# Kernel tuning notes

Measured on AMD Instinct MI355X. Metric: run time of the kernel, lower is better.

## Reference

```python
import jax, jax.numpy as jnp
import numpy as np

N_TOKEN = 267735
CUTOFF_ENDS = [0, 20000, 40000, 200000, N_TOKEN]
DIV_VAL = 4
D_MODEL = 1024
N_HEAD = 16
D_HEAD = 64
D_INNER = 4096
N_LAYER = 4
QLEN = 512
MLEN = 512
BSZ = 4
EPS = 1e-5


def setup_inputs() -> dict:
    key = jax.random.key(0)
    ks = iter(jax.random.split(key, 40))
    std = 0.02
    inp = {}
    inp["input_ids"] = jax.random.randint(next(ks), (BSZ, QLEN), 0, N_TOKEN)
    inp["mems"] = jax.random.normal(next(ks), (N_LAYER, MLEN, BSZ, D_MODEL), jnp.float32) * std
    # adaptive embedding tables + projections (div_val=4 buckets)
    for i in range(4):
        n = CUTOFF_ENDS[i + 1] - CUTOFF_ENDS[i]
        d = D_MODEL // DIV_VAL ** i
        inp[f"emb{i}"] = jax.random.normal(next(ks), (n, d), jnp.float32) * std
        inp[f"proj{i}"] = jax.random.normal(next(ks), (d, D_MODEL), jnp.float32) * std
    L = N_LAYER
    inp["qkv_w"] = jax.random.normal(next(ks), (L, D_MODEL, 3 * N_HEAD * D_HEAD), jnp.float32) * std
    inp["r_net_w"] = jax.random.normal(next(ks), (L, D_MODEL, N_HEAD * D_HEAD), jnp.float32) * std
    inp["o_w"] = jax.random.normal(next(ks), (L, N_HEAD * D_HEAD, D_MODEL), jnp.float32) * std
    inp["r_w_bias"] = jax.random.normal(next(ks), (L, N_HEAD, D_HEAD), jnp.float32) * std
    inp["r_r_bias"] = jax.random.normal(next(ks), (L, N_HEAD, D_HEAD), jnp.float32) * std
    inp["ln1_g"] = jnp.ones((L, D_MODEL), jnp.float32)
    inp["ln1_b"] = jnp.zeros((L, D_MODEL), jnp.float32)
    inp["ff_w1"] = jax.random.normal(next(ks), (L, D_MODEL, D_INNER), jnp.float32) * std
    inp["ff_b1"] = jnp.zeros((L, D_INNER), jnp.float32)
    inp["ff_w2"] = jax.random.normal(next(ks), (L, D_INNER, D_MODEL), jnp.float32) * std
    inp["ff_b2"] = jnp.zeros((L, D_MODEL), jnp.float32)
    inp["ln2_g"] = jnp.ones((L, D_MODEL), jnp.float32)
    inp["ln2_b"] = jnp.zeros((L, D_MODEL), jnp.float32)
    return inp


def _layer_norm(x, g, b):
    m = x.mean(-1, keepdims=True)
    v = ((x - m) ** 2).mean(-1, keepdims=True)
    return (x - m) * jax.lax.rsqrt(v + EPS) * g + b


def _rel_shift(x):
    # x: (qlen, klen, bsz, n_head)
    q, k, b, n = x.shape
    x = jnp.pad(x, ((0, 0), (1, 0), (0, 0), (0, 0)))
    x = x.reshape(k + 1, q, b, n)[1:]
    return x.reshape(q, k, b, n)


def _adaptive_embed(flat_ids, tables_projs):
    emb = jnp.zeros((flat_ids.shape[0], D_MODEL), jnp.float32)
    for i, (tab, proj) in enumerate(tables_projs):
        l, r = CUTOFF_ENDS[i], CUTOFF_ENDS[i + 1]
        mask = (flat_ids >= l) & (flat_ids < r)
        idx = jnp.clip(flat_ids - l, 0, r - l - 1)
        emb = emb + jnp.where(mask[:, None], tab[idx] @ proj, 0.0)
    return emb * (D_MODEL ** 0.5)


def _forward(input_ids, mems, tables_projs, qkv_w, r_net_w, o_w, r_w_bias, r_r_bias,
             ln1_g, ln1_b, ff_w1, ff_b1, ff_w2, ff_b2, ln2_g, ln2_b):
    ids = input_ids.T  # (qlen, bsz)
    word_emb = _adaptive_embed(ids.reshape(-1), tables_projs).reshape(QLEN, BSZ, D_MODEL)

    klen = MLEN + QLEN
    # masked positions == 1: future tokens only (strictly upper triangular over the q part)
    dec_attn_mask = jnp.concatenate(
        [jnp.zeros((QLEN, MLEN), jnp.float32), jnp.triu(jnp.ones((QLEN, QLEN), jnp.float32), 1)], axis=1
    )[:, :, None, None]  # (qlen, klen, 1, 1)

    pos_seq = jnp.arange(klen - 1, -1, -1, dtype=jnp.float32)
    inv_freq = 1.0 / (10000.0 ** (jnp.arange(0, D_MODEL, 2, dtype=jnp.float32) / D_MODEL))
    sin_inp = pos_seq[:, None] * inv_freq[None, :]
    pos_emb = jnp.concatenate([jnp.sin(sin_inp), jnp.cos(sin_inp)], axis=-1)  # (klen, d_model)

    scale = 1.0 / (D_HEAD ** 0.5)
    h = word_emb
    for l in range(N_LAYER):
        cat = jnp.concatenate([mems[l], h], axis=0)              # (klen, bsz, d)
        w_heads = cat @ qkv_w[l]                                  # (klen, bsz, 3*nh*dh)
        wq, wk, wv = jnp.split(w_heads, 3, axis=-1)
        q = wq[-QLEN:].reshape(QLEN, BSZ, N_HEAD, D_HEAD)
        k = wk.reshape(klen, BSZ, N_HEAD, D_HEAD)
        v = wv.reshape(klen, BSZ, N_HEAD, D_HEAD)
        rk = (pos_emb @ r_net_w[l]).reshape(klen, N_HEAD, D_HEAD)
        AC = jnp.einsum('ibnd,jbnd->ijbn', q + r_w_bias[l], k)
        BD = _rel_shift(jnp.einsum('ibnd,jnd->ijbn', q + r_r_bias[l], rk))
        score = (AC + BD) * scale
        score = score * (1.0 - dec_attn_mask) - 1e30 * dec_attn_mask
        prob = jax.nn.softmax(score, axis=1)
        attn_vec = jnp.einsum('ijbn,jbnd->ibnd', prob, v).reshape(QLEN, BSZ, N_HEAD * D_HEAD)
        h = _layer_norm(h + attn_vec @ o_w[l], ln1_g[l], ln1_b[l])
        core = jax.nn.relu(h @ ff_w1[l] + ff_b1[l]) @ ff_w2[l] + ff_b2[l]
        h = _layer_norm(h + core, ln2_g[l], ln2_b[l])
    return jnp.transpose(h, (1, 0, 2))  # (bsz, qlen, d_model)


def reference(input_ids, mems, emb0, proj0, emb1, proj1, emb2, proj2, emb3, proj3,
              qkv_w, r_net_w, o_w, r_w_bias, r_r_bias, ln1_g, ln1_b,
              ff_w1, ff_b1, ff_w2, ff_b2, ln2_g, ln2_b):
    tables_projs = [(emb0, proj0), (emb1, proj1), (emb2, proj2), (emb3, proj3)]
    return _forward(input_ids, mems, tables_projs, qkv_w, r_net_w, o_w, r_w_bias, r_r_bias,
                    ln1_g, ln1_b, ff_w1, ff_b1, ff_w2, ff_b2, ln2_g, ln2_b)
```

## Files before the change

### kernel.cpp

```cpp
#include <hip/hip_runtime.h>
#include <hip/hip_bf16.h>

typedef __attribute__((ext_vector_type(8))) short short8;
typedef __attribute__((ext_vector_type(4))) float f32x4;
typedef __hip_bfloat16 bf16;

#define QLEN 512
#define MLEN 512
#define KLEN 1024
#define BSZ  4
#define DM   1024
#define NH   16
#define DH   64
#define DI   4096
#define NL   4
#define KEMB 1408

__device__ __forceinline__ void gload16(const bf16* g, const void* l) {
  __builtin_amdgcn_global_load_lds(
      (const __attribute__((address_space(1))) void*)g,
      (__attribute__((address_space(3))) void*)l, 16, 0, 0);
}

__device__ __forceinline__ bf16 bits2bf(short s) { bf16 h; *(short*)&h = s; return h; }

__global__ __launch_bounds__(256) void embA_kernel(
    const int* __restrict__ ids,
    const float* __restrict__ e0, const float* __restrict__ e1,
    const float* __restrict__ e2, const float* __restrict__ e3,
    bf16* __restrict__ Aemb)
{
  const int t = blockIdx.x;
  const int q = t >> 2, b = t & 3;
  const int id = ids[b * QLEN + q];
  const float* tab; int d, off, koff;
  if (id < 20000)       { tab = e0; d = 1024; off = 0;      koff = 0; }
  else if (id < 40000)  { tab = e1; d = 256;  off = 20000;  koff = 1024; }
  else if (id < 200000) { tab = e2; d = 64;   off = 40000;  koff = 1280; }
  else                  { tab = e3; d = 16;   off = 200000; koff = 1344; }
  bf16* row = Aemb + (long)t * KEMB;
  const float* tr = tab + (long)(id - off) * d;
  for (int k = threadIdx.x; k < KEMB; k += 256) {
    const int kk = k - koff;
    float v = 0.f;
    if (kk >= 0 && kk < d) v = tr[kk];
    row[k] = __float2bfloat16(v);
  }
}

__global__ __launch_bounds__(256) void projT_kernel(
    const float* __restrict__ p0, const float* __restrict__ p1,
    const float* __restrict__ p2, const float* __restrict__ p3,
    bf16* __restrict__ out)
{
  __shared__ float t[32][33];
  const int k0 = blockIdx.x * 32, n0 = blockIdx.y * 32;
  const int nx = threadIdx.x & 31, ky = threadIdx.x >> 5;
#pragma unroll
  for (int p = 0; p < 4; ++p) {
    const int k = k0 + ky + p * 8;
    float v = 0.f;
    if (k < 1024)       v = p0[(long)k * 1024 + n0 + nx];
    else if (k < 1280)  v = p1[(long)(k - 1024) * 1024 + n0 + nx];
    else if (k < 1344)  v = p2[(long)(k - 1280) * 1024 + n0 + nx];
    else if (k < 1360)  v = p3[(long)(k - 1344) * 1024 + n0 + nx];
    t[ky + p * 8][nx] = v;
  }
  __syncthreads();
#pragma unroll
  for (int p = 0; p < 4; ++p)
    out[(long)(n0 + ky + p * 8) * KEMB + k0 + nx] = __float2bfloat16(t[nx][ky + p * 8]);
}

__global__ __launch_bounds__(256) void embsum_kernel(const float* __restrict__ part,
                                                     float* __restrict__ h, bf16* __restrict__ cat)
{
  const long i = ((long)blockIdx.x * 256 + threadIdx.x) * 4;
  const float4 a = *(const float4*)(part + i);
  const float4 b = *(const float4*)(part + 2097152 + i);
  float4 s; s.x = a.x + b.x; s.y = a.y + b.y; s.z = a.z + b.z; s.w = a.w + b.w;
  *(float4*)(h + i) = s;
  bf16* cr = cat + (long)2048 * 1024 + i;
  cr[0] = __float2bfloat16(s.x); cr[1] = __float2bfloat16(s.y);
  cr[2] = __float2bfloat16(s.z); cr[3] = __float2bfloat16(s.w);
}

__global__ __launch_bounds__(256) void posemb_kernel(bf16* __restrict__ pe)
{
  const int j = blockIdx.x;
  const float pos = (float)(KLEN - 1 - j);
  for (int i = threadIdx.x; i < DM / 2; i += 256) {
    const float freq = expf(-9.210340371976184f * ((float)(2 * i) / (float)DM));
    const float ang = pos * freq;
    pe[(long)j * DM + i]          = __float2bfloat16(sinf(ang));
    pe[(long)j * DM + DM / 2 + i] = __float2bfloat16(cosf(ang));
  }
}

__global__ __launch_bounds__(256) void wtrans_kernel(const float* __restrict__ in,
                                                     bf16* __restrict__ out, int R, int C)
{
  __shared__ float t[32][33];
  in  += (long)blockIdx.z * R * C;
  out += (long)blockIdx.z * R * C;
  const int c0 = blockIdx.x * 32, r0 = blockIdx.y * 32;
  const int cx = threadIdx.x & 31, ry = threadIdx.x >> 5;
#pragma unroll
  for (int p = 0; p < 4; ++p)
    t[ry + p * 8][cx] = in[(long)(r0 + ry + p * 8) * C + c0 + cx];
  __syncthreads();
#pragma unroll
  for (int p = 0; p < 4; ++p)
    out[(long)(c0 + ry + p * 8) * R + r0 + cx] = __float2bfloat16(t[cx][ry + p * 8]);
}

__global__ __launch_bounds__(256) void memsconv_kernel(const float* __restrict__ mems,
                                                       bf16* __restrict__ cat0)
{
  const long i = ((long)blockIdx.x * 256 + threadIdx.x) * 4;
  const long l = i >> 21, rem = i & ((1 << 21) - 1);
  const float4 v = *(const float4*)(mems + i);
  bf16* dst = cat0 + l * 4194304 + rem;
  dst[0] = __float2bfloat16(v.x); dst[1] = __float2bfloat16(v.y);
  dst[2] = __float2bfloat16(v.z); dst[3] = __float2bfloat16(v.w);
}

template<int BM, int BN>
__global__ __launch_bounds__(256) void gemm_bf16(
    const bf16* __restrict__ A, long aStrB, long aStrN, int lda,
    const bf16* __restrict__ B, long bStrB, long bStrN, int ldb,
    void* __restrict__ C, long cStrB, long cStrN, int ldc,
    int K, float scale, const float* __restrict__ bias, long biasStrB, long biasStrN,
    int flags, int zN, int zSplit, long cSplitStr)
{
  constexpr int RA = BM / 64, RB = BN / 64, FM = BM / 32, FN = BN / 32;
  __shared__ __align__(16) bf16 As[2][BM * 32];
  __shared__ __align__(16) bf16 Bs[2][BN * 32];
  const int zc = blockIdx.z % zSplit, zt = blockIdx.z / zSplit;
  const int zn = zt % zN, zb = zt / zN;
  A += (long)zb * aStrB + (long)zn * aStrN + (long)zc * K;
  B += (long)zb * bStrB + (long)zn * bStrN + (long)zc * K;
  const int tid = threadIdx.x, lane = tid & 63;
  const int w = tid >> 6, wr = w >> 1, wc = w & 1;
  const int m0 = blockIdx.y * BM, n0 = blockIdx.x * BN;
  const int l15 = lane & 15, l4 = lane >> 4;
  const int rowS = tid >> 2;
  const int cbS  = (tid & 3) * 16;
  const int swS  = cbS ^ (((rowS >> 1) & 3) << 4);
  const int wbase = w * 1024;
  const bf16* Ast = A + (size_t)(m0 + rowS) * lda + (swS >> 1);
  const bf16* Bst = B + (size_t)(n0 + rowS) * ldb + (swS >> 1);

#define STAGE_TILE(buf, kk)                                                       \
  {                                                                               \
    _Pragma("unroll")                                                             \
    for (int r = 0; r < RA; ++r)                                                  \
      gload16(Ast + (size_t)(r * 64) * lda + (kk), (char*)As[buf] + r * 4096 + wbase); \
    _Pragma("unroll")                                                             \
    for (int r = 0; r < RB; ++r)                                                  \
      gload16(Bst + (size_t)(r * 64) * ldb + (kk), (char*)Bs[buf] + r * 4096 + wbase); \
  }

  f32x4 acc[FM][FN] = {};
  STAGE_TILE(0, 0)
  asm volatile("s_waitcnt vmcnt(0)" ::: "memory");
  __syncthreads();
  int cur = 0;
  for (int k0 = 0; k0 < K; k0 += 32) {
    if (k0 + 32 < K) {
      if (cur == 0) STAGE_TILE(1, k0 + 32)
      else          STAGE_TILE(0, k0 + 32)
    }
    short8 af[FM], bfr[FN];
#pragma unroll
    for (int f = 0; f < FM; ++f) {
      const int row = wr * (BM / 2) + f * 16 + l15;
      af[f] = *(const short8*)((char*)As[cur] + row * 64 + ((16 * l4) ^ (((row >> 1) & 3) << 4)));
    }
#pragma unroll
    for (int f = 0; f < FN; ++f) {
      const int row = wc * (BN / 2) + f * 16 + l15;
      bfr[f] = *(const short8*)((char*)Bs[cur] + row * 64 + ((16 * l4) ^ (((row >> 1) & 3) << 4)));
    }
#pragma unroll
    for (int fm = 0; fm < FM; ++fm)
#pragma unroll
      for (int fn = 0; fn < FN; ++fn)
        acc[fm][fn] = __builtin_amdgcn_mfma_f32_16x16x32_bf16(af[fm], bfr[fn], acc[fm][fn], 0, 0, 0);
    asm volatile("s_waitcnt vmcnt(0)" ::: "memory");
    __syncthreads();
    cur ^= 1;
  }
#undef STAGE_TILE
  const int outbf = flags & 1, relu = flags & 4;
#pragma unroll
  for (int fm = 0; fm < FM; ++fm) {
#pragma unroll
    for (int fn = 0; fn < FN; ++fn) {
      const int col = n0 + wc * (BN / 2) + fn * 16 + l15;
      const int rw0 = m0 + wr * (BM / 2) + fm * 16 + l4 * 4;
      const float bv = (bias && zc == 0) ? bias[(size_t)zb * biasStrB + (size_t)zn * biasStrN + col] : 0.f;
#pragma unroll
      for (int r = 0; r < 4; ++r) {
        float v = (acc[fm][fn][r] + bv) * scale;
        if (relu) v = fmaxf(v, 0.f);
        const int row = rw0 + r;
        const size_t cOff = (size_t)zb * cStrB + (size_t)zn * cStrN + (size_t)zc * cSplitStr;
        if (outbf) {
          ((bf16*)C + cOff)[(size_t)row * ldc + col] = __float2bfloat16(v);
        } else {
          ((float*)C + cOff)[(size_t)row * ldc + col] = v;
        }
      }
    }
  }
}

__global__ __launch_bounds__(256) void vt_kernel(const bf16* __restrict__ wh,
                                                 bf16* __restrict__ vt, bf16* __restrict__ kb)
{
  const int bn = blockIdx.y, b = bn >> 4, n = bn & 15;
  const int j0 = blockIdx.x * 64;
  __shared__ bf16 t[64][72];
  const bf16* src = wh + (size_t)b * 3072 + 2048 + n * 64;
  const bf16* ksrc = wh + (size_t)b * 3072 + 1024 + n * 64;
  bf16* kdst = kb + (size_t)bn * 65536;
  const int tid = threadIdx.x;
#pragma unroll
  for (int r = 0; r < 16; ++r) {
    const int jl = r * 4 + (tid >> 6), d = tid & 63;
    t[jl][d] = src[(size_t)(j0 + jl) * 12288 + d];
    kdst[(size_t)(j0 + jl) * 64 + d] = ksrc[(size_t)(j0 + jl) * 12288 + d];
  }
  __syncthreads();
  bf16* dst = vt + (size_t)bn * 64 * KLEN;
#pragma unroll
  for (int r = 0; r < 16; ++r) {
    const int d = r * 4 + (tid >> 6), j = tid & 63;
    dst[(size_t)d * KLEN + j0 + j] = t[j][d];
  }
}

__global__ __launch_bounds__(256) void fattn_kernel(
    const bf16* __restrict__ wh,
    const bf16* __restrict__ kb,
    const bf16* __restrict__ rkb_l,
    const bf16* __restrict__ vt,
    const float* __restrict__ rwb,
    const float* __restrict__ rrb,
    float* __restrict__ po, float* __restrict__ pm, float* __restrict__ pl)
{
  const int bn = blockIdx.x, b = bn >> 4, n = bn & 15;
  const int q0 = blockIdx.y * 64;
  const int ck = blockIdx.z;
  const int tid = threadIdx.x, w = tid >> 6, lane = tid & 63;
  const int l15 = lane & 15, l4 = lane >> 4;
  __shared__ bf16 Tl[4][16][84];
  __shared__ bf16 Pl[4][16][72];

  short8 qa[2], qb[2];
  {
    const bf16* qp = wh + (size_t)(2048 + b) * 3072 + (size_t)(q0 + 16 * w + l15) * 12288 + n * 64;
#pragma unroll
    for (int kk = 0; kk < 2; ++kk) {
      const short8 qv = *(const short8*)(qp + kk * 32 + 8 * l4);
      const float* wv = rwb + n * 64 + kk * 32 + 8 * l4;
      const float* rv = rrb + n * 64 + kk * 32 + 8 * l4;
      short8 a, c;
#pragma unroll
      for (int e = 0; e < 8; ++e) {
        const float q = __bfloat162float(bits2bf(qv[e]));
        const bf16 ab = __float2bfloat16((q + wv[e]) * 0.125f);
        const bf16 cb = __float2bfloat16((q + rv[e]) * 0.125f);
        a[e] = *(const short*)&ab;  c[e] = *(const short*)&cb;
      }
      qa[kk] = a; qb[kk] = c;
    }
  }

  const bf16* kbase = kb + (size_t)bn * 65536;
  const bf16* vbase = vt + (size_t)bn * 65536;
  const int ntiles = 9 + (q0 >> 6);
  const int pb0 = -q0 + 496 - 16 * w;

  f32x4 accO[4] = {};
  float mrow[4] = { -1e30f, -1e30f, -1e30f, -1e30f };
  float lrow[4] = { 0.f, 0.f, 0.f, 0.f };

  for (int t = ck; t < ntiles; t += 4) {
    const int j0 = t * 64;
    f32x4 S[4] = {};
    __builtin_amdgcn_s_setprio(1);
#pragma unroll
    for (int fn = 0; fn < 4; ++fn)
#pragma unroll
      for (int kk = 0; kk < 2; ++kk) {
        const short8 kf = *(const short8*)(kbase + (size_t)(j0 + 16 * fn + l15) * 64 + kk * 32 + 8 * l4);
        S[fn] = __builtin_amdgcn_mfma_f32_16x16x32_bf16(qa[kk], kf, S[fn], 0, 0, 0);
      }
    {
      f32x4 T[5] = {};
#pragma unroll
      for (int ftl = 0; ftl < 5; ++ftl) {
        const int p = pb0 + j0 + 16 * ftl + l15;
#pragma unroll
        for (int kk = 0; kk < 2; ++kk) {
          const short8 rf = *(const short8*)(rkb_l + (size_t)p * 1024 + n * 64 + kk * 32 + 8 * l4);
          T[ftl] = __builtin_amdgcn_mfma_f32_16x16x32_bf16(qb[kk], rf, T[ftl], 0, 0, 0);
        }
      }
      __builtin_amdgcn_s_setprio(0);
#pragma unroll
      for (int ftl = 0; ftl < 5; ++ftl)
#pragma unroll
        for (int r = 0; r < 4; ++r)
          Tl[w][4 * l4 + r][16 * ftl + l15] = __float2bfloat16(T[ftl][r]);
    }
    const bool fullvalid = (j0 + 63) <= (512 + q0);
    float sv[4][4];
#pragma unroll
    for (int fn = 0; fn < 4; ++fn)
#pragma unroll
      for (int r = 0; r < 4; ++r) {
        const int il = 4 * l4 + r;
        const float tshift = __bfloat162float(Tl[w][il][16 * fn + l15 + 15 - il]);
        const float s = S[fn][r] + tshift;
        const bool valid = fullvalid || (j0 + 16 * fn + l15 - 512 <= q0 + 16 * w + il);
        sv[fn][r] = valid ? s : -1e30f;
      }
    float pv[4][4];
#pragma unroll
    for (int r = 0; r < 4; ++r) {
      float m4 = fmaxf(fmaxf(sv[0][r], sv[1][r]), fmaxf(sv[2][r], sv[3][r]));
      m4 = fmaxf(m4, __shfl_xor(m4, 1));
      m4 = fmaxf(m4, __shfl_xor(m4, 2));
      m4 = fmaxf(m4, __shfl_xor(m4, 4));
      m4 = fmaxf(m4, __shfl_xor(m4, 8));
      const float mn = fmaxf(mrow[r], m4);
      const float alpha = expf(mrow[r] - mn);
      mrow[r] = mn;
      float ps = 0.f;
#pragma unroll
      for (int fn = 0; fn < 4; ++fn) {
        const float e = expf(sv[fn][r] - mn);
        pv[fn][r] = e; ps += e;
      }
      ps += __shfl_xor(ps, 1);
      ps += __shfl_xor(ps, 2);
      ps += __shfl_xor(ps, 4);
      ps += __shfl_xor(ps, 8);
      lrow[r] = lrow[r] * alpha + ps;
#pragma unroll
      for (int fd = 0; fd < 4; ++fd) accO[fd][r] *= alpha;
    }
#pragma unroll
    for (int fn = 0; fn < 4; ++fn)
#pragma unroll
      for (int r = 0; r < 4; ++r)
        Pl[w][4 * l4 + r][16 * fn + l15] = __float2bfloat16(pv[fn][r]);
    short8 pa[2];
    pa[0] = *(const short8*)&Pl[w][l15][8 * l4];
    pa[1] = *(const short8*)&Pl[w][l15][32 + 8 * l4];
    __builtin_amdgcn_s_setprio(1);
#pragma unroll
    for (int fd = 0; fd < 4; ++fd)
#pragma unroll
      for (int kk = 0; kk < 2; ++kk) {
        const short8 vf = *(const short8*)(vbase + (size_t)(16 * fd + l15) * 1024 + j0 + kk * 32 + 8 * l4);
        accO[fd] = __builtin_amdgcn_mfma_f32_16x16x32_bf16(pa[kk], vf, accO[fd], 0, 0, 0);
      }
    __builtin_amdgcn_s_setprio(0);
  }
  const int cb = ck * 64 + bn;
  float* pob = po + (size_t)cb * 512 * 64;
#pragma unroll
  for (int fd = 0; fd < 4; ++fd)
#pragma unroll
    for (int r = 0; r < 4; ++r) {
      const int row = q0 + 16 * w + 4 * l4 + r;
      pob[(size_t)row * 64 + 16 * fd + l15] = accO[fd][r];
    }
  if (l15 == 0) {
#pragma unroll
    for (int r = 0; r < 4; ++r) {
      const int row = q0 + 16 * w + 4 * l4 + r;
      pm[(size_t)cb * 512 + row] = mrow[r];
      pl[(size_t)cb * 512 + row] = lrow[r];
    }
  }
}

__global__ __launch_bounds__(256) void fmerge_kernel(
    const float* __restrict__ po, const float* __restrict__ pm,
    const float* __restrict__ pl, bf16* __restrict__ av)
{
  const long i = ((long)blockIdx.x * 256 + threadIdx.x) * 4;
  const long bnq = i >> 6;
  const int d4 = (int)(i & 63);
  const int bn = (int)(bnq >> 9), q = (int)(bnq & 511);
  const int b = bn >> 4, n = bn & 15;
  float mv[4], lv[4];
#pragma unroll
  for (int c = 0; c < 4; ++c) { mv[c] = pm[c * 32768 + bnq]; lv[c] = pl[c * 32768 + bnq]; }
  const float m = fmaxf(fmaxf(mv[0], mv[1]), fmaxf(mv[2], mv[3]));
  float wv[4], den = 0.f;
#pragma unroll
  for (int c = 0; c < 4; ++c) { wv[c] = expf(mv[c] - m); den += wv[c] * lv[c]; }
  const float inv = 1.f / den;
  float4 o = { 0.f, 0.f, 0.f, 0.f };
#pragma unroll
  for (int c = 0; c < 4; ++c) {
    const float4 oc = *(const float4*)(po + (size_t)c * 2097152 + bnq * 64 + d4);
    o.x += wv[c] * oc.x; o.y += wv[c] * oc.y; o.z += wv[c] * oc.z; o.w += wv[c] * oc.w;
  }
  bf16* dst = av + (size_t)(q * 4 + b) * 1024 + n * 64 + d4;
  dst[0] = __float2bfloat16(o.x * inv);
  dst[1] = __float2bfloat16(o.y * inv);
  dst[2] = __float2bfloat16(o.z * inv);
  dst[3] = __float2bfloat16(o.w * inv);
}

__global__ __launch_bounds__(256) void add_ln_kernel(
    float* __restrict__ h,
    const float* __restrict__ x0, const float* __restrict__ x1,
    const float* __restrict__ g, const float* __restrict__ bb, bf16* __restrict__ cat)
{
  float* hr = h + (long)blockIdx.x * DM;
  const long o = (long)blockIdx.x * DM;
  bf16* cr = cat + (long)(2048 + blockIdx.x) * DM;
  const int tid = threadIdx.x;
  __shared__ float red[256];
  float v0 = hr[tid]       + x0[o + tid]       + x1[o + tid];
  float v1 = hr[tid + 256] + x0[o + tid + 256] + x1[o + tid + 256];
  float v2 = hr[tid + 512] + x0[o + tid + 512] + x1[o + tid + 512];
  float v3 = hr[tid + 768] + x0[o + tid + 768] + x1[o + tid + 768];
  red[tid] = v0 + v1 + v2 + v3; __syncthreads();
  for (int off = 128; off; off >>= 1) { if (tid < off) red[tid] += red[tid + off]; __syncthreads(); }
  const float mean = red[0] * (1.f / DM); __syncthreads();
  const float d0 = v0 - mean, d1 = v1 - mean, d2 = v2 - mean, d3 = v3 - mean;
  red[tid] = d0 * d0 + d1 * d1 + d2 * d2 + d3 * d3; __syncthreads();
  for (int off = 128; off; off >>= 1) { if (tid < off) red[tid] += red[tid + off]; __syncthreads(); }
  const float inv = rsqrtf(red[0] * (1.f / DM) + 1e-5f);
  const float o0 = d0 * inv * g[tid]       + bb[tid];
  const float o1 = d1 * inv * g[tid + 256] + bb[tid + 256];
  const float o2 = d2 * inv * g[tid + 512] + bb[tid + 512];
  const float o3 = d3 * inv * g[tid + 768] + bb[tid + 768];
  hr[tid]       = o0;  cr[tid]       = __float2bfloat16(o0);
  hr[tid + 256] = o1;  cr[tid + 256] = __float2bfloat16(o1);
  hr[tid + 512] = o2;  cr[tid + 512] = __float2bfloat16(o2);
  hr[tid + 768] = o3;  cr[tid + 768] = __float2bfloat16(o3);
}

__global__ __launch_bounds__(256) void out_kernel(const float* __restrict__ h, float* __restrict__ out)
{
  const int t = blockIdx.x, q = t >> 2, b = t & 3;
  const float* hr = h + (long)t * DM;
  float* orow = out + ((long)b * QLEN + q) * DM;
  for (int s = 0; s < 4; ++s) orow[threadIdx.x + 256 * s] = hr[threadIdx.x + 256 * s];
}

extern "C" void kernel_launch(void* const* d_in, const int* in_sizes, int n_in,
                              void* d_out, int out_size, void* d_ws, size_t ws_size,
                              hipStream_t stream)
{
  const int*   ids  = (const int*)d_in[0];
  const float* mems = (const float*)d_in[1];
  const float* e0 = (const float*)d_in[2]; const float* p0 = (const float*)d_in[3];
  const float* e1 = (const float*)d_in[4]; const float* p1 = (const float*)d_in[5];
  const float* e2 = (const float*)d_in[6]; const float* p2 = (const float*)d_in[7];
  const float* e3 = (const float*)d_in[8]; const float* p3 = (const float*)d_in[9];
  const float* qkvw = (const float*)d_in[10];
  const float* rnet = (const float*)d_in[11];
  const float* ow   = (const float*)d_in[12];
  const float* rwb  = (const float*)d_in[13];
  const float* rrb  = (const float*)d_in[14];
  const float* ln1g = (const float*)d_in[15];
  const float* ln1b = (const float*)d_in[16];
  const float* fw1  = (const float*)d_in[17];
  const float* fb1  = (const float*)d_in[18];
  const float* fw2  = (const float*)d_in[19];
  const float* fb2  = (const float*)d_in[20];
  const float* ln2g = (const float*)d_in[21];
  const float* ln2b = (const float*)d_in[22];
  float* out = (float*)d_out;

  char* p = (char*)d_ws;
  float* h    = (float*)p;            p += (size_t)2048 * 1024 * 4;
  bf16*  cat0 = (bf16*)p;             p += (size_t)5 * 4096 * 1024 * 2;
  bf16*  pe   = (bf16*)p;             p += (size_t)1024 * 1024 * 2;
  bf16*  rkb  = (bf16*)p;             p += (size_t)4 * 1024 * 1024 * 2;
  bf16*  wh   = (bf16*)p;             p += (size_t)4096 * 3072 * 2;
  bf16*  vt   = (bf16*)p;             p += (size_t)64 * 64 * 1024 * 2;
  bf16*  kb   = (bf16*)p;             p += (size_t)64 * 1024 * 64 * 2;
  bf16*  qkvT = (bf16*)p;             p += (size_t)4 * 3072 * 1024 * 2;
  bf16*  rnT  = (bf16*)p;             p += (size_t)4 * 1024 * 1024 * 2;
  bf16*  oT   = (bf16*)p;             p += (size_t)4 * 1024 * 1024 * 2;
  bf16*  f1T  = (bf16*)p;             p += (size_t)4 * 4096 * 1024 * 2;
  bf16*  f2T  = (bf16*)p;             p += (size_t)4 * 4096 * 1024 * 2;
  bf16*  mid  = (bf16*)p;
  float* partE= (float*)p;
  p += (size_t)4 * 16 * 512 * 1024 * 2;
  bf16*  Aemb = (bf16*)p;
  bf16*  projT= (bf16*)(p + (size_t)2048 * KEMB * 2);
  float* partP= (float*)p;
  float* po   = (float*)p;
  float* pm   = (float*)(p + (size_t)32 * 1024 * 1024);
  float* pl   = (float*)(p + (size_t)33 * 1024 * 1024);
  p += (size_t)4 * 16 * 512 * 1024 * 2;
  bf16*  av   = (bf16*)p;             p += (size_t)2048 * 1024 * 2;

  embA_kernel<<<2048, 256, 0, stream>>>(ids, e0, e1, e2, e3, Aemb);
  projT_kernel<<<dim3(KEMB / 32, 32), 256, 0, stream>>>(p0, p1, p2, p3, projT);
  gemm_bf16<128, 64><<<dim3(16, 16, 2), 256, 0, stream>>>(
      Aemb, 0, 0, KEMB, projT, 0, 0, KEMB, partE, 0, 0, 1024,
      KEMB / 2, 32.f, nullptr, 0, 0, 0, 1, 2, 2097152);
  embsum_kernel<<<2048, 256, 0, stream>>>(partE, h, cat0);
  posemb_kernel<<<1024, 256, 0, stream>>>(pe);
  memsconv_kernel<<<8192, 256, 0, stream>>>(mems, cat0);

  wtrans_kernel<<<dim3(96, 32, 4), 256, 0, stream>>>(qkvw, qkvT, DM, 3072);
  wtrans_kernel<<<dim3(32, 32, 4), 256, 0, stream>>>(rnet, rnT, DM, DM);
  wtrans_kernel<<<dim3(32, 32, 4), 256, 0, stream>>>(ow, oT, DM, DM);
  wtrans_kernel<<<dim3(128, 32, 4), 256, 0, stream>>>(fw1, f1T, DM, DI);
  wtrans_kernel<<<dim3(32, 128, 4), 256, 0, stream>>>(fw2, f2T, DI, DM);

  gemm_bf16<128, 128><<<dim3(8, 8, 4), 256, 0, stream>>>(
      pe, 0, 0, 1024, rnT, 1048576, 0, 1024, rkb, 1048576, 0, 1024,
      1024, 1.f, nullptr, 0, 0, 1, 1, 1, 0);

  for (int l = 0; l < NL; ++l) {
    bf16* catl = cat0 + (size_t)l * 4194304;
    gemm_bf16<128, 128><<<dim3(24, 32, 1), 256, 0, stream>>>(
        catl, 0, 0, 1024, qkvT + (size_t)l * 3145728, 0, 0, 1024, wh, 0, 0, 3072,
        1024, 1.f, nullptr, 0, 0, 1, 1, 1, 0);

    vt_kernel<<<dim3(16, 64), 256, 0, stream>>>(wh, vt, kb);

    fattn_kernel<<<dim3(64, 8, 4), 256, 0, stream>>>(
        wh, kb, rkb + (size_t)l * 1048576, vt,
        rwb + l * NH * DH, rrb + l * NH * DH, po, pm, pl);
    fmerge_kernel<<<2048, 256, 0, stream>>>(po, pm, pl, av);

    gemm_bf16<128, 64><<<dim3(16, 16, 2), 256, 0, stream>>>(
        av, 0, 0, 1024, oT + (size_t)l * 1048576, 0, 0, 1024, partP, 0, 0, 1024,
        512, 1.f, nullptr, 0, 0, 0, 1, 2, 2097152);
    add_ln_kernel<<<2048, 256, 0, stream>>>(h, partP, partP + 2097152,
                                            ln1g + l * DM, ln1b + l * DM, catl);

    gemm_bf16<128, 128><<<dim3(32, 16, 1), 256, 0, stream>>>(
        catl + (size_t)2048 * 1024, 0, 0, 1024, f1T + (size_t)l * 4194304, 0, 0, 1024,
        mid, 0, 0, 4096, 1024, 1.f, fb1 + (size_t)l * DI, 0, 0, 1 | 4, 1, 1, 0);
    gemm_bf16<128, 64><<<dim3(16, 16, 2), 256, 0, stream>>>(
        mid, 0, 0, 4096, f2T + (size_t)l * 4194304, 0, 0, 4096, partP, 0, 0, 1024,
        2048, 1.f, fb2 + (size_t)l * DM, 0, 0, 0, 1, 2, 2097152);
    add_ln_kernel<<<2048, 256, 0, stream>>>(h, partP, partP + 2097152,
                                            ln2g + l * DM, ln2b + l * DM,
                                            cat0 + (size_t)(l + 1) * 4194304);
  }

  out_kernel<<<2048, 256, 0, stream>>>(h, out);
}
```

Before: 1.136 ms.

## Repack V and relative keys into per-head contiguous tiles for attention

```diff
diff --git a/kernel.cpp b/kernel.cpp
--- a/kernel.cpp
+++ b/kernel.cpp
@@ -233,18 +233,33 @@
     kdst[(size_t)(j0 + jl) * 64 + d] = ksrc[(size_t)(j0 + jl) * 12288 + d];
   }
   __syncthreads();
-  bf16* dst = vt + (size_t)bn * 64 * KLEN;
+  bf16* dst = vt + (size_t)bn * 65536 + (size_t)j0 * 64;
 #pragma unroll
   for (int r = 0; r < 16; ++r) {
     const int d = r * 4 + (tid >> 6), j = tid & 63;
-    dst[(size_t)d * KLEN + j0 + j] = t[j][d];
+    dst[(size_t)d * 64 + j] = t[j][d];
+  }
+}
+
+__global__ __launch_bounds__(256) void rkpack_kernel(const bf16* __restrict__ rkb,
+                                                     bf16* __restrict__ rkn)
+{
+  const int ln = blockIdx.y, l = ln >> 4, n = ln & 15;
+  const int p0 = blockIdx.x * 64;
+  const int d = threadIdx.x & 63, pr = threadIdx.x >> 6;
+  const bf16* src = rkb + (size_t)l * 1048576 + n * 64 + d;
+  bf16* dst = rkn + (size_t)ln * 65536 + d;
+#pragma unroll
+  for (int r = 0; r < 16; ++r) {
+    const int p = p0 + r * 4 + pr;
+    dst[(size_t)p * 64] = src[(size_t)p * 1024];
   }
 }
 
 __global__ __launch_bounds__(256) void fattn_kernel(
     const bf16* __restrict__ wh,
     const bf16* __restrict__ kb,
-    const bf16* __restrict__ rkb_l,
+    const bf16* __restrict__ rkn_l,
     const bf16* __restrict__ vt,
     const float* __restrict__ rwb,
     const float* __restrict__ rrb,
@@ -279,6 +294,7 @@
   }
 
   const bf16* kbase = kb + (size_t)bn * 65536;
+  const bf16* rbase = rkn_l + (size_t)n * 65536;
   const bf16* vbase = vt + (size_t)bn * 65536;
   const int ntiles = 9 + (q0 >> 6);
   const int pb0 = -q0 + 496 - 16 * w;
@@ -290,7 +306,6 @@
   for (int t = ck; t < ntiles; t += 4) {
     const int j0 = t * 64;
     f32x4 S[4] = {};
-    __builtin_amdgcn_s_setprio(1);
 #pragma unroll
     for (int fn = 0; fn < 4; ++fn)
 #pragma unroll
@@ -305,11 +320,10 @@
         const int p = pb0 + j0 + 16 * ftl + l15;
 #pragma unroll
         for (int kk = 0; kk < 2; ++kk) {
-          const short8 rf = *(const short8*)(rkb_l + (size_t)p * 1024 + n * 64 + kk * 32 + 8 * l4);
+          const short8 rf = *(const short8*)(rbase + (size_t)p * 64 + kk * 32 + 8 * l4);
           T[ftl] = __builtin_amdgcn_mfma_f32_16x16x32_bf16(qb[kk], rf, T[ftl], 0, 0, 0);
         }
       }
-      __builtin_amdgcn_s_setprio(0);
 #pragma unroll
       for (int ftl = 0; ftl < 5; ++ftl)
 #pragma unroll
@@ -328,7 +342,6 @@
         const bool valid = fullvalid || (j0 + 16 * fn + l15 - 512 <= q0 + 16 * w + il);
         sv[fn][r] = valid ? s : -1e30f;
       }
-    float pv[4][4];
 #pragma unroll
     for (int r = 0; r < 4; ++r) {
       float m4 = fmaxf(fmaxf(sv[0][r], sv[1][r]), fmaxf(sv[2][r], sv[3][r]));
@@ -342,8 +355,8 @@
       float ps = 0.f;
 #pragma unroll
       for (int fn = 0; fn < 4; ++fn) {
-        const float e = expf(sv[fn][r] - mn);
-        pv[fn][r] = e; ps += e;
+        sv[fn][r] = expf(sv[fn][r] - mn);
+        ps += sv[fn][r];
       }
       ps += __shfl_xor(ps, 1);
       ps += __shfl_xor(ps, 2);
@@ -357,19 +370,18 @@
     for (int fn = 0; fn < 4; ++fn)
 #pragma unroll
       for (int r = 0; r < 4; ++r)
-        Pl[w][4 * l4 + r][16 * fn + l15] = __float2bfloat16(pv[fn][r]);
+        Pl[w][4 * l4 + r][16 * fn + l15] = __float2bfloat16(sv[fn][r]);
     short8 pa[2];
     pa[0] = *(const short8*)&Pl[w][l15][8 * l4];
     pa[1] = *(const short8*)&Pl[w][l15][32 + 8 * l4];
-    __builtin_amdgcn_s_setprio(1);
+    const bf16* vtile = vbase + (size_t)j0 * 64;
 #pragma unroll
     for (int fd = 0; fd < 4; ++fd)
 #pragma unroll
       for (int kk = 0; kk < 2; ++kk) {
-        const short8 vf = *(const short8*)(vbase + (size_t)(16 * fd + l15) * 1024 + j0 + kk * 32 + 8 * l4);
+        const short8 vf = *(const short8*)(vtile + (size_t)(16 * fd + l15) * 64 + kk * 32 + 8 * l4);
         accO[fd] = __builtin_amdgcn_mfma_f32_16x16x32_bf16(pa[kk], vf, accO[fd], 0, 0, 0);
       }
-    __builtin_amdgcn_s_setprio(0);
   }
   const int cb = ck * 64 + bn;
   float* pob = po + (size_t)cb * 512 * 64;
@@ -489,6 +501,7 @@
   bf16*  cat0 = (bf16*)p;             p += (size_t)5 * 4096 * 1024 * 2;
   bf16*  pe   = (bf16*)p;             p += (size_t)1024 * 1024 * 2;
   bf16*  rkb  = (bf16*)p;             p += (size_t)4 * 1024 * 1024 * 2;
+  bf16*  rkn  = (bf16*)p;             p += (size_t)(4 * 16 * 1024 * 64 + 8192) * 2;
   bf16*  wh   = (bf16*)p;             p += (size_t)4096 * 3072 * 2;
   bf16*  vt   = (bf16*)p;             p += (size_t)64 * 64 * 1024 * 2;
   bf16*  kb   = (bf16*)p;             p += (size_t)64 * 1024 * 64 * 2;
@@ -527,6 +540,7 @@
   gemm_bf16<128, 128><<<dim3(8, 8, 4), 256, 0, stream>>>(
       pe, 0, 0, 1024, rnT, 1048576, 0, 1024, rkb, 1048576, 0, 1024,
       1024, 1.f, nullptr, 0, 0, 1, 1, 1, 0);
+  rkpack_kernel<<<dim3(16, 64), 256, 0, stream>>>(rkb, rkn);
 
   for (int l = 0; l < NL; ++l) {
     bf16* catl = cat0 + (size_t)l * 4194304;
@@ -537,7 +551,7 @@
     vt_kernel<<<dim3(16, 64), 256, 0, stream>>>(wh, vt, kb);
 
     fattn_kernel<<<dim3(64, 8, 4), 256, 0, stream>>>(
-        wh, kb, rkb + (size_t)l * 1048576, vt,
+        wh, kb, rkn + (size_t)l * 1048576, vt,
         rwb + l * NH * DH, rrb + l * NH * DH, po, pm, pl);
     fmerge_kernel<<<2048, 256, 0, stream>>>(po, pm, pl, av);
 
```

Result: no change. 1.159 ms (+2.0%).
